# Kernel tuning notes

Hardware: AMD Instinct MI355X
Metric: run time of the kernel (lower is better)

The kernel has to match this reference:

```python
import jax, jax.numpy as jnp
import numpy as np

N_NODES = 50000
N_EDGES = 600000
D_IN = 128
HID = 128
N_SAGE = 2          # num_layers - 1
N_GRAPHS = 512
BN_EPS = 1e-5


def setup_inputs() -> dict:
    key = jax.random.key(0)
    ks = jax.random.split(key, 12)
    s = 1.0 / np.sqrt(HID)
    x = jax.random.normal(ks[0], (N_NODES, D_IN), dtype=jnp.float32)
    edge_index = jax.random.randint(ks[1], (2, N_EDGES), 0, N_NODES, dtype=jnp.int32)
    batch = jnp.sort(jax.random.randint(ks[2], (N_NODES,), 0, N_GRAPHS, dtype=jnp.int32))
    # GIN MLP: Linear(D_IN,HID) -> ReLU -> Linear(HID,HID)
    gin_w1 = jax.random.normal(ks[3], (D_IN, HID), dtype=jnp.float32) * s
    gin_b1 = jnp.zeros((HID,), jnp.float32)
    gin_w2 = jax.random.normal(ks[4], (HID, HID), dtype=jnp.float32) * s
    gin_b2 = jnp.zeros((HID,), jnp.float32)
    # SAGEConv layers: lin_l (neighbors, with bias), lin_r (root, no bias)
    sage_wl = jax.random.normal(ks[5], (N_SAGE, HID, HID), dtype=jnp.float32) * s
    sage_bl = jnp.zeros((N_SAGE, HID), jnp.float32)
    sage_wr = jax.random.normal(ks[6], (N_SAGE, HID, HID), dtype=jnp.float32) * s
    # BatchNorm per layer (3 layers)
    bn_gamma = jnp.ones((1 + N_SAGE, HID), jnp.float32)
    bn_beta = jnp.zeros((1 + N_SAGE, HID), jnp.float32)
    return {"x": x, "edge_index": edge_index, "batch": batch,
            "gin_w1": gin_w1, "gin_b1": gin_b1, "gin_w2": gin_w2, "gin_b2": gin_b2,
            "sage_wl": sage_wl, "sage_bl": sage_bl, "sage_wr": sage_wr,
            "bn_gamma": bn_gamma, "bn_beta": bn_beta}


def _batchnorm(h, gamma, beta):
    # training-mode BN over the node dimension (biased variance, as torch)
    mu = jnp.mean(h, axis=0)
    var = jnp.var(h, axis=0)
    return gamma * (h - mu) * jax.lax.rsqrt(var + BN_EPS) + beta


def reference(x, edge_index, batch, gin_w1, gin_b1, gin_w2, gin_b2,
              sage_wl, sage_bl, sage_wr, bn_gamma, bn_beta):
    n = x.shape[0]
    src, dst = edge_index[0], edge_index[1]

    # ---- Layer 0: GINConv (eps=0): mlp(x + sum_{j->i} x_j) ----
    agg = jax.ops.segment_sum(x[src], dst, num_segments=n)  # [N, D_IN]
    h = x + agg
    h = jax.nn.relu(h @ gin_w1 + gin_b1) @ gin_w2 + gin_b2
    h = jax.nn.relu(_batchnorm(h, bn_gamma[0], bn_beta[0]))
    # dropout is identity (eval mode)

    # degree for mean aggregation (shared across SAGE layers)
    deg = jax.ops.segment_sum(jnp.ones((src.shape[0],), h.dtype), dst, num_segments=n)
    inv_deg = (1.0 / jnp.maximum(deg, 1.0))[:, None]  # [N,1]

    # ---- SAGE layers: lin_l(mean_{j->i} h_j) + lin_r(h_i) ----
    for l in range(N_SAGE):
        neigh = jax.ops.segment_sum(h[src], dst, num_segments=n) * inv_deg
        h = neigh @ sage_wl[l] + sage_bl[l] + h @ sage_wr[l]
        h = jax.nn.relu(_batchnorm(h, bn_gamma[l + 1], bn_beta[l + 1]))

    # ---- global mean pool over batch ids ----
    sums = jax.ops.segment_sum(h, batch, num_segments=N_GRAPHS)  # [G, HID]
    counts = jax.ops.segment_sum(jnp.ones((n,), h.dtype), batch, num_segments=N_GRAPHS)
    return sums / jnp.maximum(counts, 1.0)[:, None]
```

## Files before the change

### kernel.cpp

```cpp
#include <hip/hip_runtime.h>

#define N_NODES 50000
#define N_EDGES 600000
#define HID 128
#define N_GRAPHS 512
#define BN_EPS 1e-5f
#define INV_N (1.0f / 50000.0f)

typedef __attribute__((ext_vector_type(8))) short bf16x8;
typedef __attribute__((ext_vector_type(4))) float f32x4;

__device__ __forceinline__ unsigned short f2b(float f) {
    unsigned u = __float_as_uint(f);
    return (unsigned short)((u + 0x7FFFu + ((u >> 16) & 1u)) >> 16);
}
__device__ __forceinline__ float b2f(unsigned short h) {
    return __uint_as_float(((unsigned)h) << 16);
}

#define CONVX_BLOCKS 6250
#define WCONV_BLOCKS 384
#define DEG_BLOCKS   2344
__global__ __launch_bounds__(256) void prep_kernel(
    const float* __restrict__ x, const float* __restrict__ gw1, const float* __restrict__ gw2,
    const float* __restrict__ swl, const float* __restrict__ swr, const int* __restrict__ dst,
    unsigned short* __restrict__ x16, unsigned short* __restrict__ wt, int* __restrict__ deg)
{
    int b = blockIdx.x;
    int t = threadIdx.x;
    if (b < CONVX_BLOCKS) {
        int gid = b * 256 + t;
        int i = gid >> 5, l = gid & 31;
        if (i >= N_NODES) return;
        int c0 = l * 4;
        float4 v = *(const float4*)(x + (size_t)i * 128 + c0);
        ushort4 o;
        o.x = f2b(v.x); o.y = f2b(v.y); o.z = f2b(v.z); o.w = f2b(v.w);
        *(ushort4*)(x16 + (size_t)i * 128 + c0) = o;
    } else if (b < CONVX_BLOCKS + WCONV_BLOCKS) {
        int gid = (b - CONVX_BLOCKS) * 256 + t;
        int m = gid >> 14;
        int e = gid & 16383;
        int k = e >> 7;
        int n = e & 127;
        const float* src = (m == 0) ? gw1 : (m == 1) ? gw2 : (m == 2) ? swl
                         : (m == 3) ? swr : (m == 4) ? (swl + 16384) : (swr + 16384);
        wt[m * 16384 + n * 128 + k] = f2b(src[k * 128 + n]);
    } else {
        int e = (b - CONVX_BLOCKS - WCONV_BLOCKS) * 256 + t;
        if (e < N_EDGES) atomicAdd(&deg[dst[e]], 1);
    }
}

#define ALLOC_BLOCKS 196
__global__ __launch_bounds__(256) void alloc_kernel(int* __restrict__ cursor,
                                                    int* __restrict__ row_beg,
                                                    float* __restrict__ inv_deg,
                                                    int* __restrict__ total,
                                                    const int* __restrict__ batch,
                                                    int* __restrict__ gstart) {
    if (blockIdx.x >= ALLOC_BLOCKS) {
        int g = (blockIdx.x - ALLOC_BLOCKS) * 256 + threadIdx.x;
        if (g > N_GRAPHS) return;
        int lo = 0, hi = N_NODES;
        while (lo < hi) {
            int mid = (lo + hi) >> 1;
            if (batch[mid] < g) lo = mid + 1; else hi = mid;
        }
        gstart[g] = lo;
        return;
    }
    __shared__ int tmp[256];
    __shared__ int base;
    int i = blockIdx.x * 256 + threadIdx.x;
    int d = (i < N_NODES) ? cursor[i] : 0;
    tmp[threadIdx.x] = d;
    __syncthreads();
#pragma unroll
    for (int off = 1; off < 256; off <<= 1) {
        int v = (threadIdx.x >= off) ? tmp[threadIdx.x - off] : 0;
        __syncthreads();
        tmp[threadIdx.x] += v;
        __syncthreads();
    }
    if (threadIdx.x == 255) base = atomicAdd(total, tmp[255]);
    __syncthreads();
    if (i < N_NODES) {
        int b = base + tmp[threadIdx.x] - d;
        row_beg[i] = b;
        cursor[i] = b;
        inv_deg[i] = 1.0f / fmaxf((float)d, 1.0f);
    }
}

__global__ void csr_fill_kernel(const int* __restrict__ src, const int* __restrict__ dst,
                                int* __restrict__ cursor, unsigned short* __restrict__ csr_src, int nE) {
    int e = blockIdx.x * blockDim.x + threadIdx.x;
    if (e < nE) {
        int pos = atomicAdd(&cursor[dst[e]], 1);
        csr_src[pos] = (unsigned short)src[e];
    }
}

#define IDXCAP 2048
template<bool AFF, bool MEAN, bool HACT>
__global__ __launch_bounds__(256) void aggregate_kernel(
    const unsigned short* __restrict__ feat,
    const int* __restrict__ row_beg, const int* __restrict__ row_end,
    const unsigned short* __restrict__ csr_src,
    const float* __restrict__ stats, const float* __restrict__ gamma,
    const float* __restrict__ beta, const float* __restrict__ inv_deg,
    unsigned short* __restrict__ agg, unsigned short* __restrict__ hact, int n)
{
    __shared__ unsigned short idxbuf[IDXCAP];
    const int t = threadIdx.x;
    const int node0 = blockIdx.x * 16;
    const int node = node0 + (t >> 4);
    const int lane = t & 15;
    const int c0 = lane * 8;

    const int last = (node0 + 15 < n) ? node0 + 15 : n - 1;
    const int ebeg = row_beg[node0];
    const int ecnt = row_end[last] - ebeg;
    const bool lds_ok = (ecnt <= IDXCAP);
    if (lds_ok) {
        for (int i = t; i < ecnt; i += 256) idxbuf[i] = csr_src[ebeg + i];
    }
    __syncthreads();
    if (node >= n) return;

    float cc[8], ss[8];
    if (AFF) {
#pragma unroll
        for (int j = 0; j < 8; j++) {
            int col = c0 + j;
            float mu = stats[col] * INV_N;
            float var = stats[128 + col] * INV_N - mu * mu;
            float rs = rsqrtf(var + BN_EPS);
            float c = gamma[col] * rs;
            cc[j] = c;
            ss[j] = beta[col] - mu * c;
        }
    }

    float a[8];
#pragma unroll
    for (int j = 0; j < 8; j++) a[j] = 0.f;

    const int beg = row_beg[node];
    const int deg = row_end[node] - beg;

    if (lds_ok) {
        const int off = beg - ebeg;
        int e = 0;
        for (; e + 7 < deg; e += 8) {
            int s[8];
#pragma unroll
            for (int u = 0; u < 8; u++) s[u] = idxbuf[off + e + u];
            bf16x8 v[8];
#pragma unroll
            for (int u = 0; u < 8; u++)
                v[u] = *(const bf16x8*)(feat + (size_t)s[u] * 128 + c0);
#pragma unroll
            for (int u = 0; u < 8; u++) {
#pragma unroll
                for (int j = 0; j < 8; j++) {
                    float tv = b2f((unsigned short)v[u][j]);
                    if (AFF) tv = fmaxf(tv * cc[j] + ss[j], 0.f);
                    a[j] += tv;
                }
            }
        }
        for (; e + 3 < deg; e += 4) {
            int s[4];
#pragma unroll
            for (int u = 0; u < 4; u++) s[u] = idxbuf[off + e + u];
            bf16x8 v[4];
#pragma unroll
            for (int u = 0; u < 4; u++)
                v[u] = *(const bf16x8*)(feat + (size_t)s[u] * 128 + c0);
#pragma unroll
            for (int u = 0; u < 4; u++) {
#pragma unroll
                for (int j = 0; j < 8; j++) {
                    float tv = b2f((unsigned short)v[u][j]);
                    if (AFF) tv = fmaxf(tv * cc[j] + ss[j], 0.f);
                    a[j] += tv;
                }
            }
        }
        for (; e < deg; e++) {
            int s0 = idxbuf[off + e];
            bf16x8 v0 = *(const bf16x8*)(feat + (size_t)s0 * 128 + c0);
#pragma unroll
            for (int j = 0; j < 8; j++) {
                float tv = b2f((unsigned short)v0[j]);
                if (AFF) tv = fmaxf(tv * cc[j] + ss[j], 0.f);
                a[j] += tv;
            }
        }
    } else {
        int e = beg, end = beg + deg;
        for (; e + 3 < end; e += 4) {
            int s0 = csr_src[e];
            int s1 = csr_src[e + 1];
            int s2 = csr_src[e + 2];
            int s3 = csr_src[e + 3];
            bf16x8 v0 = *(const bf16x8*)(feat + (size_t)s0 * 128 + c0);
            bf16x8 v1 = *(const bf16x8*)(feat + (size_t)s1 * 128 + c0);
            bf16x8 v2 = *(const bf16x8*)(feat + (size_t)s2 * 128 + c0);
            bf16x8 v3 = *(const bf16x8*)(feat + (size_t)s3 * 128 + c0);
#pragma unroll
            for (int j = 0; j < 8; j++) {
                float t0 = b2f((unsigned short)v0[j]);
                float t1 = b2f((unsigned short)v1[j]);
                float t2 = b2f((unsigned short)v2[j]);
                float t3 = b2f((unsigned short)v3[j]);
                if (AFF) {
                    t0 = fmaxf(t0 * cc[j] + ss[j], 0.f);
                    t1 = fmaxf(t1 * cc[j] + ss[j], 0.f);
                    t2 = fmaxf(t2 * cc[j] + ss[j], 0.f);
                    t3 = fmaxf(t3 * cc[j] + ss[j], 0.f);
                }
                a[j] += (t0 + t1) + (t2 + t3);
            }
        }
        for (; e < end; e++) {
            int s0 = csr_src[e];
            bf16x8 v0 = *(const bf16x8*)(feat + (size_t)s0 * 128 + c0);
#pragma unroll
            for (int j = 0; j < 8; j++) {
                float t0 = b2f((unsigned short)v0[j]);
                if (AFF) t0 = fmaxf(t0 * cc[j] + ss[j], 0.f);
                a[j] += t0;
            }
        }
    }

    if (MEAN) {
        float s = inv_deg[node];
#pragma unroll
        for (int j = 0; j < 8; j++) a[j] *= s;
    }
    bf16x8 o;
#pragma unroll
    for (int j = 0; j < 8; j++) o[j] = (short)f2b(a[j]);
    *(bf16x8*)(agg + (size_t)node * 128 + c0) = o;

    if (HACT) {
        bf16x8 v = *(const bf16x8*)(feat + (size_t)node * 128 + c0);
        bf16x8 h;
#pragma unroll
        for (int j = 0; j < 8; j++)
            h[j] = (short)f2b(fmaxf(b2f((unsigned short)v[j]) * cc[j] + ss[j], 0.f));
        *(bf16x8*)(hact + (size_t)node * 128 + c0) = h;
    }
}

__global__ __launch_bounds__(256, 2) void gemm_gin_kernel(
    const unsigned short* __restrict__ X, const unsigned short* __restrict__ AGG,
    const unsigned short* __restrict__ W1t, const unsigned short* __restrict__ W2t,
    const float* __restrict__ b1, const float* __restrict__ b2,
    float* __restrict__ stats, unsigned short* __restrict__ Cb,
    int M, int ntiles)
{
    __shared__ unsigned short t1[32][136];
    __shared__ float red[2][128];

    const int t = threadIdx.x;
    const int wave = t >> 6;
    const int lane = t & 63;
    const int colhalf = wave & 1;
    const int rowpair = wave >> 1;
    const int m16 = lane & 15;
    const int quad = lane >> 4;
    const int k0 = quad * 8;
    const int colbase = colhalf * 64;
    const int lrow = rowpair * 16 + m16;

    const bf16x8 zero8 = {0, 0, 0, 0, 0, 0, 0, 0};

    bf16x8 w1f[4][4], w2f[4][4];
#pragma unroll
    for (int ct = 0; ct < 4; ct++) {
        int col = colbase + ct * 16 + m16;
#pragma unroll
        for (int kc = 0; kc < 4; kc++) {
            w1f[ct][kc] = *(const bf16x8*)(W1t + (size_t)col * 128 + kc * 32 + k0);
            w2f[ct][kc] = *(const bf16x8*)(W2t + (size_t)col * 128 + kc * 32 + k0);
        }
    }
    f32x4 bs1[4], bs2[4];
#pragma unroll
    for (int ct = 0; ct < 4; ct++) {
        bs1[ct] = *(const f32x4*)(b1 + colbase + ct * 16 + quad * 4);
        bs2[ct] = *(const f32x4*)(b2 + colbase + ct * 16 + quad * 4);
    }

    float psum[4][4], psq[4][4];
#pragma unroll
    for (int ct = 0; ct < 4; ct++)
#pragma unroll
        for (int r = 0; r < 4; r++) { psum[ct][r] = 0.f; psq[ct][r] = 0.f; }

    for (int tile = blockIdx.x; tile < ntiles; tile += gridDim.x) {
        int arow = tile * 32 + rowpair * 16 + m16;
        bool aok = arow < M;

        bf16x8 a[4];
#pragma unroll
        for (int kc = 0; kc < 4; kc++) {
            if (aok) {
                bf16x8 vx = *(const bf16x8*)(X + (size_t)arow * 128 + kc * 32 + k0);
                bf16x8 vg = *(const bf16x8*)(AGG + (size_t)arow * 128 + kc * 32 + k0);
                bf16x8 r;
#pragma unroll
                for (int i = 0; i < 8; i++)
                    r[i] = (short)f2b(b2f((unsigned short)vx[i]) + b2f((unsigned short)vg[i]));
                a[kc] = r;
            } else {
                a[kc] = zero8;
            }
        }

        f32x4 acc[4];
#pragma unroll
        for (int ct = 0; ct < 4; ct++) acc[ct] = (f32x4){0.f, 0.f, 0.f, 0.f};
#pragma unroll
        for (int kc = 0; kc < 4; kc++)
#pragma unroll
            for (int ct = 0; ct < 4; ct++)
                acc[ct] = __builtin_amdgcn_mfma_f32_16x16x32_bf16(w1f[ct][kc], a[kc], acc[ct], 0, 0, 0);

        __syncthreads();
#pragma unroll
        for (int ct = 0; ct < 4; ct++) {
            f32x4 v = acc[ct] + bs1[ct];
            ushort4 o;
            o.x = f2b(fmaxf(v[0], 0.f));
            o.y = f2b(fmaxf(v[1], 0.f));
            o.z = f2b(fmaxf(v[2], 0.f));
            o.w = f2b(fmaxf(v[3], 0.f));
            *(ushort4*)&t1[lrow][colbase + ct * 16 + quad * 4] = o;
        }
        __syncthreads();

        bf16x8 ta[4];
#pragma unroll
        for (int kc = 0; kc < 4; kc++)
            ta[kc] = *(const bf16x8*)&t1[lrow][kc * 32 + k0];

        f32x4 acc2[4];
#pragma unroll
        for (int ct = 0; ct < 4; ct++) acc2[ct] = (f32x4){0.f, 0.f, 0.f, 0.f};
#pragma unroll
        for (int kc = 0; kc < 4; kc++)
#pragma unroll
            for (int ct = 0; ct < 4; ct++)
                acc2[ct] = __builtin_amdgcn_mfma_f32_16x16x32_bf16(w2f[ct][kc], ta[kc], acc2[ct], 0, 0, 0);

        int orow = arow;
        if (orow < M) {
#pragma unroll
            for (int ct = 0; ct < 4; ct++) {
                f32x4 v = acc2[ct] + bs2[ct];
                int col = colbase + ct * 16 + quad * 4;
#pragma unroll
                for (int r = 0; r < 4; r++) { psum[ct][r] += v[r]; psq[ct][r] += v[r] * v[r]; }
                ushort4 o;
                o.x = f2b(v[0]); o.y = f2b(v[1]); o.z = f2b(v[2]); o.w = f2b(v[3]);
                *(ushort4*)(Cb + (size_t)orow * 128 + col) = o;
            }
        }
    }

#pragma unroll
    for (int ct = 0; ct < 4; ct++)
#pragma unroll
        for (int r = 0; r < 4; r++) {
#pragma unroll
            for (int mask = 1; mask <= 8; mask <<= 1) {
                psum[ct][r] += __shfl_xor(psum[ct][r], mask, 64);
                psq[ct][r]  += __shfl_xor(psq[ct][r], mask, 64);
            }
        }
    __syncthreads();
    if (m16 == 0) {
#pragma unroll
        for (int ct = 0; ct < 4; ct++)
#pragma unroll
            for (int r = 0; r < 4; r++)
                red[rowpair][colbase + ct * 16 + quad * 4 + r] = psum[ct][r];
    }
    __syncthreads();
    if (t < 128) atomicAdd(&stats[t], red[0][t] + red[1][t]);
    __syncthreads();
    if (m16 == 0) {
#pragma unroll
        for (int ct = 0; ct < 4; ct++)
#pragma unroll
            for (int r = 0; r < 4; r++)
                red[rowpair][colbase + ct * 16 + quad * 4 + r] = psq[ct][r];
    }
    __syncthreads();
    if (t < 128) atomicAdd(&stats[128 + t], red[0][t] + red[1][t]);
}

__global__ __launch_bounds__(256) void gemm_dual_kernel(
    const unsigned short* __restrict__ A1, const unsigned short* __restrict__ A2,
    const unsigned short* __restrict__ W1t, const unsigned short* __restrict__ W2t,
    const float* __restrict__ bias, float* __restrict__ stats,
    unsigned short* __restrict__ Cb, int M, int ntiles)
{
    __shared__ float red[128];

    const int t = threadIdx.x;
    const int wave = t >> 6;
    const int lane = t & 63;
    const int m16 = lane & 15;
    const int quad = lane >> 4;
    const int k0 = quad * 8;
    const int colbase = wave * 32;

    const bf16x8 zero8 = {0, 0, 0, 0, 0, 0, 0, 0};

    bf16x8 w1f[2][4], w2f[2][4];
#pragma unroll
    for (int ct = 0; ct < 2; ct++) {
        int col = colbase + ct * 16 + m16;
#pragma unroll
        for (int kc = 0; kc < 4; kc++) {
            w1f[ct][kc] = *(const bf16x8*)(W1t + (size_t)col * 128 + kc * 32 + k0);
            w2f[ct][kc] = *(const bf16x8*)(W2t + (size_t)col * 128 + kc * 32 + k0);
        }
    }
    f32x4 bs[2];
#pragma unroll
    for (int ct = 0; ct < 2; ct++)
        bs[ct] = *(const f32x4*)(bias + colbase + ct * 16 + quad * 4);

    float psum[2][4], psq[2][4];
#pragma unroll
    for (int ct = 0; ct < 2; ct++)
#pragma unroll
        for (int r = 0; r < 4; r++) { psum[ct][r] = 0.f; psq[ct][r] = 0.f; }

    bf16x8 a1[4], a2[4], a1n[4], a2n[4];

    int tile = blockIdx.x;
    if (tile < ntiles) {
        int arow = tile * 16 + m16;
        bool aok = arow < M;
#pragma unroll
        for (int kc = 0; kc < 4; kc++) {
            a1[kc] = aok ? *(const bf16x8*)(A1 + (size_t)arow * 128 + kc * 32 + k0) : zero8;
            a2[kc] = aok ? *(const bf16x8*)(A2 + (size_t)arow * 128 + kc * 32 + k0) : zero8;
        }
    }

    for (; tile < ntiles; tile += gridDim.x) {
        int nt = tile + gridDim.x;
        if (nt < ntiles) {
            int arow = nt * 16 + m16;
            bool aok = arow < M;
#pragma unroll
            for (int kc = 0; kc < 4; kc++) {
                a1n[kc] = aok ? *(const bf16x8*)(A1 + (size_t)arow * 128 + kc * 32 + k0) : zero8;
                a2n[kc] = aok ? *(const bf16x8*)(A2 + (size_t)arow * 128 + kc * 32 + k0) : zero8;
            }
        }

        f32x4 acc[2];
        acc[0] = (f32x4){0.f, 0.f, 0.f, 0.f};
        acc[1] = (f32x4){0.f, 0.f, 0.f, 0.f};
#pragma unroll
        for (int kc = 0; kc < 4; kc++) {
#pragma unroll
            for (int ct = 0; ct < 2; ct++) {
                acc[ct] = __builtin_amdgcn_mfma_f32_16x16x32_bf16(w1f[ct][kc], a1[kc], acc[ct], 0, 0, 0);
                acc[ct] = __builtin_amdgcn_mfma_f32_16x16x32_bf16(w2f[ct][kc], a2[kc], acc[ct], 0, 0, 0);
            }
        }

        int orow = tile * 16 + m16;
        if (orow < M) {
#pragma unroll
            for (int ct = 0; ct < 2; ct++) {
                f32x4 v = acc[ct] + bs[ct];
                int col = colbase + ct * 16 + quad * 4;
#pragma unroll
                for (int r = 0; r < 4; r++) { psum[ct][r] += v[r]; psq[ct][r] += v[r] * v[r]; }
                ushort4 o;
                o.x = f2b(v[0]); o.y = f2b(v[1]); o.z = f2b(v[2]); o.w = f2b(v[3]);
                *(ushort4*)(Cb + (size_t)orow * 128 + col) = o;
            }
        }

        if (nt < ntiles) {
            a1[0] = a1n[0]; a1[1] = a1n[1]; a1[2] = a1n[2]; a1[3] = a1n[3];
            a2[0] = a2n[0]; a2[1] = a2n[1]; a2[2] = a2n[2]; a2[3] = a2n[3];
        }
    }

#pragma unroll
    for (int ct = 0; ct < 2; ct++)
#pragma unroll
        for (int r = 0; r < 4; r++) {
#pragma unroll
            for (int mask = 1; mask <= 8; mask <<= 1) {
                psum[ct][r] += __shfl_xor(psum[ct][r], mask, 64);
                psq[ct][r]  += __shfl_xor(psq[ct][r], mask, 64);
            }
        }
    if (m16 == 0) {
#pragma unroll
        for (int ct = 0; ct < 2; ct++)
#pragma unroll
            for (int r = 0; r < 4; r++)
                red[colbase + ct * 16 + quad * 4 + r] = psum[ct][r];
    }
    __syncthreads();
    if (t < 128) atomicAdd(&stats[t], red[t]);
    __syncthreads();
    if (m16 == 0) {
#pragma unroll
        for (int ct = 0; ct < 2; ct++)
#pragma unroll
            for (int r = 0; r < 4; r++)
                red[colbase + ct * 16 + quad * 4 + r] = psq[ct][r];
    }
    __syncthreads();
    if (t < 128) atomicAdd(&stats[128 + t], red[t]);
}

__global__ __launch_bounds__(128) void pool_mean_kernel(const unsigned short* __restrict__ h,
                                                        const int* __restrict__ gstart,
                                                        const float* __restrict__ stats,
                                                        const float* __restrict__ gamma,
                                                        const float* __restrict__ beta,
                                                        float* __restrict__ out) {
    __shared__ float red[8][128];
    int g = blockIdx.x;
    int t = threadIdx.x;
    int lane = t & 15, grp = t >> 4;
    int c0 = lane * 8;
    float c[8], b[8];
#pragma unroll
    for (int j = 0; j < 8; j++) {
        int col = c0 + j;
        float mu = stats[col] * INV_N;
        float var = stats[128 + col] * INV_N - mu * mu;
        float rs = rsqrtf(var + BN_EPS);
        c[j] = gamma[col] * rs;
        b[j] = beta[col] - mu * c[j];
    }
    int beg = gstart[g];
    int end = gstart[g + 1];
    float s[8];
#pragma unroll
    for (int j = 0; j < 8; j++) s[j] = 0.f;
    for (int i = beg + grp; i < end; i += 8) {
        bf16x8 v = *(const bf16x8*)(h + (size_t)i * 128 + c0);
#pragma unroll
        for (int j = 0; j < 8; j++)
            s[j] += fmaxf(b2f((unsigned short)v[j]) * c[j] + b[j], 0.f);
    }
#pragma unroll
    for (int j = 0; j < 8; j++) red[grp][c0 + j] = s[j];
    __syncthreads();
    if (t < 16) {
        float cnt = fmaxf((float)(end - beg), 1.0f);
        int cc0 = t * 8;
#pragma unroll
        for (int j = 0; j < 8; j++) {
            float tot = 0.f;
#pragma unroll
            for (int r = 0; r < 8; r++) tot += red[r][cc0 + j];
            out[(size_t)g * 128 + cc0 + j] = tot / cnt;
        }
    }
}

extern "C" void kernel_launch(void* const* d_in, const int* in_sizes, int n_in,
                              void* d_out, int out_size, void* d_ws, size_t ws_size,
                              hipStream_t stream) {
    const float* x    = (const float*)d_in[0];
    const int*   ei   = (const int*)d_in[1];
    const int*   src  = ei;
    const int*   dst  = ei + N_EDGES;
    const int*   batch = (const int*)d_in[2];
    const float* gw1  = (const float*)d_in[3];
    const float* gb1  = (const float*)d_in[4];
    const float* gw2  = (const float*)d_in[5];
    const float* gb2  = (const float*)d_in[6];
    const float* swl  = (const float*)d_in[7];
    const float* sbl  = (const float*)d_in[8];
    const float* swr  = (const float*)d_in[9];
    const float* bng  = (const float*)d_in[10];
    const float* bnb  = (const float*)d_in[11];
    float* out = (float*)d_out;

    float* ws = (float*)d_ws;
    unsigned short* x16    = (unsigned short*)(ws + 0);
    unsigned short* agg16  = (unsigned short*)(ws + 3200000);
    unsigned short* hact16 = (unsigned short*)(ws + 6400000);
    unsigned short* hpre16 = (unsigned short*)(ws + 9600000);
    unsigned short* wt     = (unsigned short*)(ws + 12800000);
    float*          inv_deg= ws + 12850000;
    int*            row_beg= (int*)(ws + 12900000);
    int*            cursor = (int*)(ws + 12950000);
    int*            total  = cursor + 50000;
    float*          stats  = (float*)(cursor + 50001);
    unsigned short* csr_src= (unsigned short*)(ws + 13100000);
    int*            gstart = (int*)(ws + 13700000);

    const int aggr_blocks = (N_NODES + 15) / 16;
    const int ntiles32 = (N_NODES + 31) / 32;
    const int ntiles16 = (N_NODES + 15) / 16;
    const int ggrid = 512;

    hipMemsetAsync(cursor, 0, (50001 + 768) * sizeof(int), stream);

    prep_kernel<<<CONVX_BLOCKS + WCONV_BLOCKS + DEG_BLOCKS, 256, 0, stream>>>(
        x, gw1, gw2, swl, swr, dst, x16, wt, cursor);

    alloc_kernel<<<ALLOC_BLOCKS + 3, 256, 0, stream>>>(cursor, row_beg, inv_deg, total, batch, gstart);
    csr_fill_kernel<<<(N_EDGES + 255) / 256, 256, 0, stream>>>(src, dst, cursor, csr_src, N_EDGES);

    aggregate_kernel<false, false, false><<<aggr_blocks, 256, 0, stream>>>(
        x16, row_beg, cursor, csr_src, nullptr, nullptr, nullptr, nullptr, agg16, nullptr, N_NODES);
    gemm_gin_kernel<<<ggrid, 256, 0, stream>>>(
        x16, agg16, wt + 0 * 16384, wt + 1 * 16384, gb1, gb2, stats + 0, hpre16, N_NODES, ntiles32);

    aggregate_kernel<true, true, true><<<aggr_blocks, 256, 0, stream>>>(
        hpre16, row_beg, cursor, csr_src, stats + 0, bng + 0 * HID, bnb + 0 * HID, inv_deg,
        agg16, hact16, N_NODES);
    gemm_dual_kernel<<<ggrid, 256, 0, stream>>>(
        agg16, hact16, wt + 2 * 16384, wt + 3 * 16384, sbl + 0 * HID, stats + 256, hpre16, N_NODES, ntiles16);

    aggregate_kernel<true, true, true><<<aggr_blocks, 256, 0, stream>>>(
        hpre16, row_beg, cursor, csr_src, stats + 256, bng + 1 * HID, bnb + 1 * HID, inv_deg,
        agg16, hact16, N_NODES);
    gemm_dual_kernel<<<ggrid, 256, 0, stream>>>(
        agg16, hact16, wt + 4 * 16384, wt + 5 * 16384, sbl + 1 * HID, stats + 512, hpre16, N_NODES, ntiles16);

    pool_mean_kernel<<<N_GRAPHS, 128, 0, stream>>>(
        hpre16, gstart, stats + 512, bng + 2 * HID, bnb + 2 * HID, out);
}
```

Measured before the change: 348.9 us.

## Fuse neighbor aggregation with GEMM per layer and shard BN stat atomics

Merges each layer's gather-aggregate kernel with its following MFMA GEMM into one persistent kernel. Each block processes 16-node groups: it gathers neighbor rows into registers, stages them in LDS, then runs the MLP or dual SAGE GEMM directly, so the intermediate agg and hact buffers are no longer written to and re-read from global memory. BatchNorm statistic atomics are spread over 8 shard copies that readers sum back together, to reduce atomic contention. In exchange, gather and GEMM run serialized within each block, with more syncthreads per group. The GIN MLP now uses 16-row tiles, and the unrolled non-LDS fallback gather loop is reduced to a simple one-edge loop.

```diff
diff --git a/kernel.cpp b/kernel.cpp
--- a/kernel.cpp
+++ b/kernel.cpp
@@ -6,6 +6,9 @@
 #define N_GRAPHS 512
 #define BN_EPS 1e-5f
 #define INV_N (1.0f / 50000.0f)
+#define NGROUPS 3125
+#define FUSED_GRID 1024
+#define IDXCAP 2048
 
 typedef __attribute__((ext_vector_type(8))) short bf16x8;
 typedef __attribute__((ext_vector_type(4))) float f32x4;
@@ -16,6 +19,13 @@
 }
 __device__ __forceinline__ float b2f(unsigned short h) {
     return __uint_as_float(((unsigned)h) << 16);
+}
+
+__device__ __forceinline__ float stats_sum(const float* __restrict__ s, int idx) {
+    float v = 0.f;
+#pragma unroll
+    for (int r = 0; r < 8; r++) v += s[r * 256 + idx];
+    return v;
 }
 
 #define CONVX_BLOCKS 6250
@@ -102,54 +112,16 @@
     }
 }
 
-#define IDXCAP 2048
-template<bool AFF, bool MEAN, bool HACT>
-__global__ __launch_bounds__(256) void aggregate_kernel(
+template<bool AFF>
+__device__ __forceinline__ void gather_row(
     const unsigned short* __restrict__ feat,
-    const int* __restrict__ row_beg, const int* __restrict__ row_end,
     const unsigned short* __restrict__ csr_src,
-    const float* __restrict__ stats, const float* __restrict__ gamma,
-    const float* __restrict__ beta, const float* __restrict__ inv_deg,
-    unsigned short* __restrict__ agg, unsigned short* __restrict__ hact, int n)
+    const unsigned short* __restrict__ idxbuf,
+    bool lds_ok, int ebeg, int beg, int deg, int c0,
+    const float (&cc)[8], const float (&ss)[8], float (&a)[8])
 {
-    __shared__ unsigned short idxbuf[IDXCAP];
-    const int t = threadIdx.x;
-    const int node0 = blockIdx.x * 16;
-    const int node = node0 + (t >> 4);
-    const int lane = t & 15;
-    const int c0 = lane * 8;
-
-    const int last = (node0 + 15 < n) ? node0 + 15 : n - 1;
-    const int ebeg = row_beg[node0];
-    const int ecnt = row_end[last] - ebeg;
-    const bool lds_ok = (ecnt <= IDXCAP);
-    if (lds_ok) {
-        for (int i = t; i < ecnt; i += 256) idxbuf[i] = csr_src[ebeg + i];
-    }
-    __syncthreads();
-    if (node >= n) return;
-
-    float cc[8], ss[8];
-    if (AFF) {
-#pragma unroll
-        for (int j = 0; j < 8; j++) {
-            int col = c0 + j;
-            float mu = stats[col] * INV_N;
-            float var = stats[128 + col] * INV_N - mu * mu;
-            float rs = rsqrtf(var + BN_EPS);
-            float c = gamma[col] * rs;
-            cc[j] = c;
-            ss[j] = beta[col] - mu * c;
-        }
-    }
-
-    float a[8];
 #pragma unroll
     for (int j = 0; j < 8; j++) a[j] = 0.f;
-
-    const int beg = row_beg[node];
-    const int deg = row_end[node] - beg;
-
     if (lds_ok) {
         const int off = beg - ebeg;
         int e = 0;
@@ -162,14 +134,13 @@
             for (int u = 0; u < 8; u++)
                 v[u] = *(const bf16x8*)(feat + (size_t)s[u] * 128 + c0);
 #pragma unroll
-            for (int u = 0; u < 8; u++) {
+            for (int u = 0; u < 8; u++)
 #pragma unroll
                 for (int j = 0; j < 8; j++) {
                     float tv = b2f((unsigned short)v[u][j]);
                     if (AFF) tv = fmaxf(tv * cc[j] + ss[j], 0.f);
                     a[j] += tv;
                 }
-            }
         }
         for (; e + 3 < deg; e += 4) {
             int s[4];
@@ -180,14 +151,13 @@
             for (int u = 0; u < 4; u++)
                 v[u] = *(const bf16x8*)(feat + (size_t)s[u] * 128 + c0);
 #pragma unroll
-            for (int u = 0; u < 4; u++) {
+            for (int u = 0; u < 4; u++)
 #pragma unroll
                 for (int j = 0; j < 8; j++) {
                     float tv = b2f((unsigned short)v[u][j]);
                     if (AFF) tv = fmaxf(tv * cc[j] + ss[j], 0.f);
                     a[j] += tv;
                 }
-            }
         }
         for (; e < deg; e++) {
             int s0 = idxbuf[off + e];
@@ -200,218 +170,30 @@
             }
         }
     } else {
-        int e = beg, end = beg + deg;
-        for (; e + 3 < end; e += 4) {
-            int s0 = csr_src[e];
-            int s1 = csr_src[e + 1];
-            int s2 = csr_src[e + 2];
-            int s3 = csr_src[e + 3];
-            bf16x8 v0 = *(const bf16x8*)(feat + (size_t)s0 * 128 + c0);
-            bf16x8 v1 = *(const bf16x8*)(feat + (size_t)s1 * 128 + c0);
-            bf16x8 v2 = *(const bf16x8*)(feat + (size_t)s2 * 128 + c0);
-            bf16x8 v3 = *(const bf16x8*)(feat + (size_t)s3 * 128 + c0);
-#pragma unroll
-            for (int j = 0; j < 8; j++) {
-                float t0 = b2f((unsigned short)v0[j]);
-                float t1 = b2f((unsigned short)v1[j]);
-                float t2 = b2f((unsigned short)v2[j]);
-                float t3 = b2f((unsigned short)v3[j]);
-                if (AFF) {
-                    t0 = fmaxf(t0 * cc[j] + ss[j], 0.f);
-                    t1 = fmaxf(t1 * cc[j] + ss[j], 0.f);
-                    t2 = fmaxf(t2 * cc[j] + ss[j], 0.f);
-                    t3 = fmaxf(t3 * cc[j] + ss[j], 0.f);
-                }
-                a[j] += (t0 + t1) + (t2 + t3);
-            }
-        }
-        for (; e < end; e++) {
+        for (int e = beg; e < beg + deg; e++) {
             int s0 = csr_src[e];
             bf16x8 v0 = *(const bf16x8*)(feat + (size_t)s0 * 128 + c0);
 #pragma unroll
             for (int j = 0; j < 8; j++) {
-                float t0 = b2f((unsigned short)v0[j]);
-                if (AFF) t0 = fmaxf(t0 * cc[j] + ss[j], 0.f);
-                a[j] += t0;
+                float tv = b2f((unsigned short)v0[j]);
+                if (AFF) tv = fmaxf(tv * cc[j] + ss[j], 0.f);
+                a[j] += tv;
             }
         }
     }
-
-    if (MEAN) {
-        float s = inv_deg[node];
-#pragma unroll
-        for (int j = 0; j < 8; j++) a[j] *= s;
-    }
-    bf16x8 o;
-#pragma unroll
-    for (int j = 0; j < 8; j++) o[j] = (short)f2b(a[j]);
-    *(bf16x8*)(agg + (size_t)node * 128 + c0) = o;
-
-    if (HACT) {
-        bf16x8 v = *(const bf16x8*)(feat + (size_t)node * 128 + c0);
-        bf16x8 h;
-#pragma unroll
-        for (int j = 0; j < 8; j++)
-            h[j] = (short)f2b(fmaxf(b2f((unsigned short)v[j]) * cc[j] + ss[j], 0.f));
-        *(bf16x8*)(hact + (size_t)node * 128 + c0) = h;
-    }
-}
-
-__global__ __launch_bounds__(256, 2) void gemm_gin_kernel(
-    const unsigned short* __restrict__ X, const unsigned short* __restrict__ AGG,
+}
+
+__global__ __launch_bounds__(256, 2) void fused_gin_kernel(
+    const unsigned short* __restrict__ X,
+    const int* __restrict__ row_beg, const int* __restrict__ row_end,
+    const unsigned short* __restrict__ csr_src,
     const unsigned short* __restrict__ W1t, const unsigned short* __restrict__ W2t,
     const float* __restrict__ b1, const float* __restrict__ b2,
-    float* __restrict__ stats, unsigned short* __restrict__ Cb,
-    int M, int ntiles)
+    float* __restrict__ stats_out, unsigned short* __restrict__ Hout, int ngroups)
 {
-    __shared__ unsigned short t1[32][136];
-    __shared__ float red[2][128];
-
-    const int t = threadIdx.x;
-    const int wave = t >> 6;
-    const int lane = t & 63;
-    const int colhalf = wave & 1;
-    const int rowpair = wave >> 1;
-    const int m16 = lane & 15;
-    const int quad = lane >> 4;
-    const int k0 = quad * 8;
-    const int colbase = colhalf * 64;
-    const int lrow = rowpair * 16 + m16;
-
-    const bf16x8 zero8 = {0, 0, 0, 0, 0, 0, 0, 0};
-
-    bf16x8 w1f[4][4], w2f[4][4];
-#pragma unroll
-    for (int ct = 0; ct < 4; ct++) {
-        int col = colbase + ct * 16 + m16;
-#pragma unroll
-        for (int kc = 0; kc < 4; kc++) {
-            w1f[ct][kc] = *(const bf16x8*)(W1t + (size_t)col * 128 + kc * 32 + k0);
-            w2f[ct][kc] = *(const bf16x8*)(W2t + (size_t)col * 128 + kc * 32 + k0);
-        }
-    }
-    f32x4 bs1[4], bs2[4];
-#pragma unroll
-    for (int ct = 0; ct < 4; ct++) {
-        bs1[ct] = *(const f32x4*)(b1 + colbase + ct * 16 + quad * 4);
-        bs2[ct] = *(const f32x4*)(b2 + colbase + ct * 16 + quad * 4);
-    }
-
-    float psum[4][4], psq[4][4];
-#pragma unroll
-    for (int ct = 0; ct < 4; ct++)
-#pragma unroll
-        for (int r = 0; r < 4; r++) { psum[ct][r] = 0.f; psq[ct][r] = 0.f; }
-
-    for (int tile = blockIdx.x; tile < ntiles; tile += gridDim.x) {
-        int arow = tile * 32 + rowpair * 16 + m16;
-        bool aok = arow < M;
-
-        bf16x8 a[4];
-#pragma unroll
-        for (int kc = 0; kc < 4; kc++) {
-            if (aok) {
-                bf16x8 vx = *(const bf16x8*)(X + (size_t)arow * 128 + kc * 32 + k0);
-                bf16x8 vg = *(const bf16x8*)(AGG + (size_t)arow * 128 + kc * 32 + k0);
-                bf16x8 r;
-#pragma unroll
-                for (int i = 0; i < 8; i++)
-                    r[i] = (short)f2b(b2f((unsigned short)vx[i]) + b2f((unsigned short)vg[i]));
-                a[kc] = r;
-            } else {
-                a[kc] = zero8;
-            }
-        }
-
-        f32x4 acc[4];
-#pragma unroll
-        for (int ct = 0; ct < 4; ct++) acc[ct] = (f32x4){0.f, 0.f, 0.f, 0.f};
-#pragma unroll
-        for (int kc = 0; kc < 4; kc++)
-#pragma unroll
-            for (int ct = 0; ct < 4; ct++)
-                acc[ct] = __builtin_amdgcn_mfma_f32_16x16x32_bf16(w1f[ct][kc], a[kc], acc[ct], 0, 0, 0);
-
-        __syncthreads();
-#pragma unroll
-        for (int ct = 0; ct < 4; ct++) {
-            f32x4 v = acc[ct] + bs1[ct];
-            ushort4 o;
-            o.x = f2b(fmaxf(v[0], 0.f));
-            o.y = f2b(fmaxf(v[1], 0.f));
-            o.z = f2b(fmaxf(v[2], 0.f));
-            o.w = f2b(fmaxf(v[3], 0.f));
-            *(ushort4*)&t1[lrow][colbase + ct * 16 + quad * 4] = o;
-        }
-        __syncthreads();
-
-        bf16x8 ta[4];
-#pragma unroll
-        for (int kc = 0; kc < 4; kc++)
-            ta[kc] = *(const bf16x8*)&t1[lrow][kc * 32 + k0];
-
-        f32x4 acc2[4];
-#pragma unroll
-        for (int ct = 0; ct < 4; ct++) acc2[ct] = (f32x4){0.f, 0.f, 0.f, 0.f};
-#pragma unroll
-        for (int kc = 0; kc < 4; kc++)
-#pragma unroll
-            for (int ct = 0; ct < 4; ct++)
-                acc2[ct] = __builtin_amdgcn_mfma_f32_16x16x32_bf16(w2f[ct][kc], ta[kc], acc2[ct], 0, 0, 0);
-
-        int orow = arow;
-        if (orow < M) {
-#pragma unroll
-            for (int ct = 0; ct < 4; ct++) {
-                f32x4 v = acc2[ct] + bs2[ct];
-                int col = colbase + ct * 16 + quad * 4;
-#pragma unroll
-                for (int r = 0; r < 4; r++) { psum[ct][r] += v[r]; psq[ct][r] += v[r] * v[r]; }
-                ushort4 o;
-                o.x = f2b(v[0]); o.y = f2b(v[1]); o.z = f2b(v[2]); o.w = f2b(v[3]);
-                *(ushort4*)(Cb + (size_t)orow * 128 + col) = o;
-            }
-        }
-    }
-
-#pragma unroll
-    for (int ct = 0; ct < 4; ct++)
-#pragma unroll
-        for (int r = 0; r < 4; r++) {
-#pragma unroll
-            for (int mask = 1; mask <= 8; mask <<= 1) {
-                psum[ct][r] += __shfl_xor(psum[ct][r], mask, 64);
-                psq[ct][r]  += __shfl_xor(psq[ct][r], mask, 64);
-            }
-        }
-    __syncthreads();
-    if (m16 == 0) {
-#pragma unroll
-        for (int ct = 0; ct < 4; ct++)
-#pragma unroll
-            for (int r = 0; r < 4; r++)
-                red[rowpair][colbase + ct * 16 + quad * 4 + r] = psum[ct][r];
-    }
-    __syncthreads();
-    if (t < 128) atomicAdd(&stats[t], red[0][t] + red[1][t]);
-    __syncthreads();
-    if (m16 == 0) {
-#pragma unroll
-        for (int ct = 0; ct < 4; ct++)
-#pragma unroll
-            for (int r = 0; r < 4; r++)
-                red[rowpair][colbase + ct * 16 + quad * 4 + r] = psq[ct][r];
-    }
-    __syncthreads();
-    if (t < 128) atomicAdd(&stats[128 + t], red[0][t] + red[1][t]);
-}
-
-__global__ __launch_bounds__(256) void gemm_dual_kernel(
-    const unsigned short* __restrict__ A1, const unsigned short* __restrict__ A2,
-    const unsigned short* __restrict__ W1t, const unsigned short* __restrict__ W2t,
-    const float* __restrict__ bias, float* __restrict__ stats,
-    unsigned short* __restrict__ Cb, int M, int ntiles)
-{
+    __shared__ unsigned short idxbuf[IDXCAP];
+    __shared__ unsigned short aT[16][136];
+    __shared__ unsigned short t1[16][136];
     __shared__ float red[128];
 
     const int t = threadIdx.x;
@@ -421,8 +203,8 @@
     const int quad = lane >> 4;
     const int k0 = quad * 8;
     const int colbase = wave * 32;
-
-    const bf16x8 zero8 = {0, 0, 0, 0, 0, 0, 0, 0};
+    const int nslot = t >> 4;
+    const int c0 = (t & 15) * 8;
 
     bf16x8 w1f[2][4], w2f[2][4];
 #pragma unroll
@@ -434,103 +216,267 @@
             w2f[ct][kc] = *(const bf16x8*)(W2t + (size_t)col * 128 + kc * 32 + k0);
         }
     }
-    f32x4 bs[2];
+    f32x4 bs1[2], bs2[2];
+#pragma unroll
+    for (int ct = 0; ct < 2; ct++) {
+        bs1[ct] = *(const f32x4*)(b1 + colbase + ct * 16 + quad * 4);
+        bs2[ct] = *(const f32x4*)(b2 + colbase + ct * 16 + quad * 4);
+    }
+
+    float psum[2][4], psq[2][4];
 #pragma unroll
     for (int ct = 0; ct < 2; ct++)
-        bs[ct] = *(const f32x4*)(bias + colbase + ct * 16 + quad * 4);
-
-    float psum[2][4], psq[2][4];
-#pragma unroll
-    for (int ct = 0; ct < 2; ct++)
 #pragma unroll
         for (int r = 0; r < 4; r++) { psum[ct][r] = 0.f; psq[ct][r] = 0.f; }
 
-    bf16x8 a1[4], a2[4], a1n[4], a2n[4];
-
-    int tile = blockIdx.x;
-    if (tile < ntiles) {
-        int arow = tile * 16 + m16;
-        bool aok = arow < M;
-#pragma unroll
-        for (int kc = 0; kc < 4; kc++) {
-            a1[kc] = aok ? *(const bf16x8*)(A1 + (size_t)arow * 128 + kc * 32 + k0) : zero8;
-            a2[kc] = aok ? *(const bf16x8*)(A2 + (size_t)arow * 128 + kc * 32 + k0) : zero8;
-        }
-    }
-
-    for (; tile < ntiles; tile += gridDim.x) {
-        int nt = tile + gridDim.x;
-        if (nt < ntiles) {
-            int arow = nt * 16 + m16;
-            bool aok = arow < M;
-#pragma unroll
-            for (int kc = 0; kc < 4; kc++) {
-                a1n[kc] = aok ? *(const bf16x8*)(A1 + (size_t)arow * 128 + kc * 32 + k0) : zero8;
-                a2n[kc] = aok ? *(const bf16x8*)(A2 + (size_t)arow * 128 + kc * 32 + k0) : zero8;
-            }
-        }
-
+    float dcc[8], dss[8];
+#pragma unroll
+    for (int j = 0; j < 8; j++) { dcc[j] = 0.f; dss[j] = 0.f; }
+
+    for (int g = blockIdx.x; g < ngroups; g += gridDim.x) {
+        const int node0 = g * 16;
+        const int node = node0 + nslot;
+        const int ebeg = row_beg[node0];
+        const int ecnt = row_end[node0 + 15] - ebeg;
+        const bool lds_ok = (ecnt <= IDXCAP);
+        if (lds_ok)
+            for (int i = t; i < ecnt; i += 256) idxbuf[i] = csr_src[ebeg + i];
+        bf16x8 vself = *(const bf16x8*)(X + (size_t)node * 128 + c0);
+        const int beg = row_beg[node];
+        const int deg = row_end[node] - beg;
+        __syncthreads();
+
+        float a[8];
+        gather_row<false>(X, csr_src, idxbuf, lds_ok, ebeg, beg, deg, c0, dcc, dss, a);
+
+        bf16x8 arow;
+#pragma unroll
+        for (int j = 0; j < 8; j++)
+            arow[j] = (short)f2b(a[j] + b2f((unsigned short)vself[j]));
+        *(bf16x8*)&aT[nslot][c0] = arow;
+        __syncthreads();
+
+        bf16x8 af[4];
+#pragma unroll
+        for (int kc = 0; kc < 4; kc++)
+            af[kc] = *(const bf16x8*)&aT[m16][kc * 32 + k0];
         f32x4 acc[2];
         acc[0] = (f32x4){0.f, 0.f, 0.f, 0.f};
         acc[1] = (f32x4){0.f, 0.f, 0.f, 0.f};
 #pragma unroll
-        for (int kc = 0; kc < 4; kc++) {
-#pragma unroll
-            for (int ct = 0; ct < 2; ct++) {
-                acc[ct] = __builtin_amdgcn_mfma_f32_16x16x32_bf16(w1f[ct][kc], a1[kc], acc[ct], 0, 0, 0);
-                acc[ct] = __builtin_amdgcn_mfma_f32_16x16x32_bf16(w2f[ct][kc], a2[kc], acc[ct], 0, 0, 0);
-            }
-        }
-
-        int orow = tile * 16 + m16;
-        if (orow < M) {
-#pragma unroll
-            for (int ct = 0; ct < 2; ct++) {
-                f32x4 v = acc[ct] + bs[ct];
-                int col = colbase + ct * 16 + quad * 4;
-#pragma unroll
-                for (int r = 0; r < 4; r++) { psum[ct][r] += v[r]; psq[ct][r] += v[r] * v[r]; }
-                ushort4 o;
-                o.x = f2b(v[0]); o.y = f2b(v[1]); o.z = f2b(v[2]); o.w = f2b(v[3]);
-                *(ushort4*)(Cb + (size_t)orow * 128 + col) = o;
-            }
-        }
-
-        if (nt < ntiles) {
-            a1[0] = a1n[0]; a1[1] = a1n[1]; a1[2] = a1n[2]; a1[3] = a1n[3];
-            a2[0] = a2n[0]; a2[1] = a2n[1]; a2[2] = a2n[2]; a2[3] = a2n[3];
+        for (int kc = 0; kc < 4; kc++)
+#pragma unroll
+            for (int ct = 0; ct < 2; ct++)
+                acc[ct] = __builtin_amdgcn_mfma_f32_16x16x32_bf16(w1f[ct][kc], af[kc], acc[ct], 0, 0, 0);
+#pragma unroll
+        for (int ct = 0; ct < 2; ct++) {
+            f32x4 v = acc[ct] + bs1[ct];
+            ushort4 o;
+            o.x = f2b(fmaxf(v[0], 0.f));
+            o.y = f2b(fmaxf(v[1], 0.f));
+            o.z = f2b(fmaxf(v[2], 0.f));
+            o.w = f2b(fmaxf(v[3], 0.f));
+            *(ushort4*)&t1[m16][colbase + ct * 16 + quad * 4] = o;
+        }
+        __syncthreads();
+
+        bf16x8 tf[4];
+#pragma unroll
+        for (int kc = 0; kc < 4; kc++)
+            tf[kc] = *(const bf16x8*)&t1[m16][kc * 32 + k0];
+        f32x4 acc2[2];
+        acc2[0] = (f32x4){0.f, 0.f, 0.f, 0.f};
+        acc2[1] = (f32x4){0.f, 0.f, 0.f, 0.f};
+#pragma unroll
+        for (int kc = 0; kc < 4; kc++)
+#pragma unroll
+            for (int ct = 0; ct < 2; ct++)
+                acc2[ct] = __builtin_amdgcn_mfma_f32_16x16x32_bf16(w2f[ct][kc], tf[kc], acc2[ct], 0, 0, 0);
+
+        const int orow = node0 + m16;
+#pragma unroll
+        for (int ct = 0; ct < 2; ct++) {
+            f32x4 v = acc2[ct] + bs2[ct];
+            int col = colbase + ct * 16 + quad * 4;
+#pragma unroll
+            for (int r = 0; r < 4; r++) { psum[ct][r] += v[r]; psq[ct][r] += v[r] * v[r]; }
+            ushort4 o;
+            o.x = f2b(v[0]); o.y = f2b(v[1]); o.z = f2b(v[2]); o.w = f2b(v[3]);
+            *(ushort4*)(Hout + (size_t)orow * 128 + col) = o;
         }
     }
 
 #pragma unroll
     for (int ct = 0; ct < 2; ct++)
 #pragma unroll
-        for (int r = 0; r < 4; r++) {
+        for (int r = 0; r < 4; r++)
 #pragma unroll
             for (int mask = 1; mask <= 8; mask <<= 1) {
                 psum[ct][r] += __shfl_xor(psum[ct][r], mask, 64);
                 psq[ct][r]  += __shfl_xor(psq[ct][r], mask, 64);
             }
-        }
-    if (m16 == 0) {
+    __syncthreads();
+    if (m16 == 0)
 #pragma unroll
         for (int ct = 0; ct < 2; ct++)
 #pragma unroll
             for (int r = 0; r < 4; r++)
                 red[colbase + ct * 16 + quad * 4 + r] = psum[ct][r];
-    }
-    __syncthreads();
-    if (t < 128) atomicAdd(&stats[t], red[t]);
-    __syncthreads();
-    if (m16 == 0) {
+    __syncthreads();
+    if (t < 128) atomicAdd(&stats_out[(blockIdx.x & 7) * 256 + t], red[t]);
+    __syncthreads();
+    if (m16 == 0)
 #pragma unroll
         for (int ct = 0; ct < 2; ct++)
 #pragma unroll
             for (int r = 0; r < 4; r++)
                 red[colbase + ct * 16 + quad * 4 + r] = psq[ct][r];
-    }
-    __syncthreads();
-    if (t < 128) atomicAdd(&stats[128 + t], red[t]);
+    __syncthreads();
+    if (t < 128) atomicAdd(&stats_out[(blockIdx.x & 7) * 256 + 128 + t], red[t]);
+}
+
+__global__ __launch_bounds__(256, 2) void fused_sage_kernel(
+    const unsigned short* __restrict__ Hin,
+    const int* __restrict__ row_beg, const int* __restrict__ row_end,
+    const unsigned short* __restrict__ csr_src,
+    const float* __restrict__ stats_in, const float* __restrict__ gamma,
+    const float* __restrict__ beta, const float* __restrict__ inv_deg,
+    const unsigned short* __restrict__ Wlt, const unsigned short* __restrict__ Wrt,
+    const float* __restrict__ bias, float* __restrict__ stats_out,
+    unsigned short* __restrict__ Hout, int ngroups)
+{
+    __shared__ unsigned short idxbuf[IDXCAP];
+    __shared__ unsigned short aT[16][136];
+    __shared__ unsigned short hT[16][136];
+    __shared__ float red[128];
+
+    const int t = threadIdx.x;
+    const int wave = t >> 6;
+    const int lane = t & 63;
+    const int m16 = lane & 15;
+    const int quad = lane >> 4;
+    const int k0 = quad * 8;
+    const int colbase = wave * 32;
+    const int nslot = t >> 4;
+    const int c0 = (t & 15) * 8;
+
+    float cc[8], ss[8];
+#pragma unroll
+    for (int j = 0; j < 8; j++) {
+        int col = c0 + j;
+        float mu = stats_sum(stats_in, col) * INV_N;
+        float var = stats_sum(stats_in, 128 + col) * INV_N - mu * mu;
+        float rs = rsqrtf(var + BN_EPS);
+        float c = gamma[col] * rs;
+        cc[j] = c;
+        ss[j] = beta[col] - mu * c;
+    }
+
+    bf16x8 wl[2][4], wr[2][4];
+#pragma unroll
+    for (int ct = 0; ct < 2; ct++) {
+        int col = colbase + ct * 16 + m16;
+#pragma unroll
+        for (int kc = 0; kc < 4; kc++) {
+            wl[ct][kc] = *(const bf16x8*)(Wlt + (size_t)col * 128 + kc * 32 + k0);
+            wr[ct][kc] = *(const bf16x8*)(Wrt + (size_t)col * 128 + kc * 32 + k0);
+        }
+    }
+    f32x4 bs[2];
+#pragma unroll
+    for (int ct = 0; ct < 2; ct++)
+        bs[ct] = *(const f32x4*)(bias + colbase + ct * 16 + quad * 4);
+
+    float psum[2][4], psq[2][4];
+#pragma unroll
+    for (int ct = 0; ct < 2; ct++)
+#pragma unroll
+        for (int r = 0; r < 4; r++) { psum[ct][r] = 0.f; psq[ct][r] = 0.f; }
+
+    for (int g = blockIdx.x; g < ngroups; g += gridDim.x) {
+        const int node0 = g * 16;
+        const int node = node0 + nslot;
+        const int ebeg = row_beg[node0];
+        const int ecnt = row_end[node0 + 15] - ebeg;
+        const bool lds_ok = (ecnt <= IDXCAP);
+        if (lds_ok)
+            for (int i = t; i < ecnt; i += 256) idxbuf[i] = csr_src[ebeg + i];
+        bf16x8 vself = *(const bf16x8*)(Hin + (size_t)node * 128 + c0);
+        const float sc = inv_deg[node];
+        const int beg = row_beg[node];
+        const int deg = row_end[node] - beg;
+        __syncthreads();
+
+        float a[8];
+        gather_row<true>(Hin, csr_src, idxbuf, lds_ok, ebeg, beg, deg, c0, cc, ss, a);
+
+        bf16x8 arow, hrow;
+#pragma unroll
+        for (int j = 0; j < 8; j++) {
+            arow[j] = (short)f2b(a[j] * sc);
+            hrow[j] = (short)f2b(fmaxf(b2f((unsigned short)vself[j]) * cc[j] + ss[j], 0.f));
+        }
+        *(bf16x8*)&aT[nslot][c0] = arow;
+        *(bf16x8*)&hT[nslot][c0] = hrow;
+        __syncthreads();
+
+        bf16x8 a1[4], a2[4];
+#pragma unroll
+        for (int kc = 0; kc < 4; kc++) {
+            a1[kc] = *(const bf16x8*)&aT[m16][kc * 32 + k0];
+            a2[kc] = *(const bf16x8*)&hT[m16][kc * 32 + k0];
+        }
+        f32x4 acc[2];
+        acc[0] = (f32x4){0.f, 0.f, 0.f, 0.f};
+        acc[1] = (f32x4){0.f, 0.f, 0.f, 0.f};
+#pragma unroll
+        for (int kc = 0; kc < 4; kc++)
+#pragma unroll
+            for (int ct = 0; ct < 2; ct++) {
+                acc[ct] = __builtin_amdgcn_mfma_f32_16x16x32_bf16(wl[ct][kc], a1[kc], acc[ct], 0, 0, 0);
+                acc[ct] = __builtin_amdgcn_mfma_f32_16x16x32_bf16(wr[ct][kc], a2[kc], acc[ct], 0, 0, 0);
+            }
+
+        const int orow = node0 + m16;
+#pragma unroll
+        for (int ct = 0; ct < 2; ct++) {
+            f32x4 v = acc[ct] + bs[ct];
+            int col = colbase + ct * 16 + quad * 4;
+#pragma unroll
+            for (int r = 0; r < 4; r++) { psum[ct][r] += v[r]; psq[ct][r] += v[r] * v[r]; }
+            ushort4 o;
+            o.x = f2b(v[0]); o.y = f2b(v[1]); o.z = f2b(v[2]); o.w = f2b(v[3]);
+            *(ushort4*)(Hout + (size_t)orow * 128 + col) = o;
+        }
+    }
+
+#pragma unroll
+    for (int ct = 0; ct < 2; ct++)
+#pragma unroll
+        for (int r = 0; r < 4; r++)
+#pragma unroll
+            for (int mask = 1; mask <= 8; mask <<= 1) {
+                psum[ct][r] += __shfl_xor(psum[ct][r], mask, 64);
+                psq[ct][r]  += __shfl_xor(psq[ct][r], mask, 64);
+            }
+    __syncthreads();
+    if (m16 == 0)
+#pragma unroll
+        for (int ct = 0; ct < 2; ct++)
+#pragma unroll
+            for (int r = 0; r < 4; r++)
+                red[colbase + ct * 16 + quad * 4 + r] = psum[ct][r];
+    __syncthreads();
+    if (t < 128) atomicAdd(&stats_out[(blockIdx.x & 7) * 256 + t], red[t]);
+    __syncthreads();
+    if (m16 == 0)
+#pragma unroll
+        for (int ct = 0; ct < 2; ct++)
+#pragma unroll
+            for (int r = 0; r < 4; r++)
+                red[colbase + ct * 16 + quad * 4 + r] = psq[ct][r];
+    __syncthreads();
+    if (t < 128) atomicAdd(&stats_out[(blockIdx.x & 7) * 256 + 128 + t], red[t]);
 }
 
 __global__ __launch_bounds__(128) void pool_mean_kernel(const unsigned short* __restrict__ h,
@@ -548,8 +494,8 @@
 #pragma unroll
     for (int j = 0; j < 8; j++) {
         int col = c0 + j;
-        float mu = stats[col] * INV_N;
-        float var = stats[128 + col] * INV_N - mu * mu;
+        float mu = stats_sum(stats, col) * INV_N;
+        float var = stats_sum(stats, 128 + col) * INV_N - mu * mu;
         float rs = rsqrtf(var + BN_EPS);
         c[j] = gamma[col] * rs;
         b[j] = beta[col] - mu * c[j];
@@ -602,9 +548,8 @@
 
     float* ws = (float*)d_ws;
     unsigned short* x16    = (unsigned short*)(ws + 0);
-    unsigned short* agg16  = (unsigned short*)(ws + 3200000);
-    unsigned short* hact16 = (unsigned short*)(ws + 6400000);
-    unsigned short* hpre16 = (unsigned short*)(ws + 9600000);
+    unsigned short* h_a    = (unsigned short*)(ws + 3200000);
+    unsigned short* h_b    = (unsigned short*)(ws + 6400000);
     unsigned short* wt     = (unsigned short*)(ws + 12800000);
     float*          inv_deg= ws + 12850000;
     int*            row_beg= (int*)(ws + 12900000);
@@ -614,12 +559,7 @@
     unsigned short* csr_src= (unsigned short*)(ws + 13100000);
     int*            gstart = (int*)(ws + 13700000);
 
-    const int aggr_blocks = (N_NODES + 15) / 16;
-    const int ntiles32 = (N_NODES + 31) / 32;
-    const int ntiles16 = (N_NODES + 15) / 16;
-    const int ggrid = 512;
-
-    hipMemsetAsync(cursor, 0, (50001 + 768) * sizeof(int), stream);
+    hipMemsetAsync(cursor, 0, (50001 + 3 * 8 * 256) * sizeof(int), stream);
 
     prep_kernel<<<CONVX_BLOCKS + WCONV_BLOCKS + DEG_BLOCKS, 256, 0, stream>>>(
         x, gw1, gw2, swl, swr, dst, x16, wt, cursor);
@@ -627,23 +567,18 @@
     alloc_kernel<<<ALLOC_BLOCKS + 3, 256, 0, stream>>>(cursor, row_beg, inv_deg, total, batch, gstart);
     csr_fill_kernel<<<(N_EDGES + 255) / 256, 256, 0, stream>>>(src, dst, cursor, csr_src, N_EDGES);
 
-    aggregate_kernel<false, false, false><<<aggr_blocks, 256, 0, stream>>>(
-        x16, row_beg, cursor, csr_src, nullptr, nullptr, nullptr, nullptr, agg16, nullptr, N_NODES);
-    gemm_gin_kernel<<<ggrid, 256, 0, stream>>>(
-        x16, agg16, wt + 0 * 16384, wt + 1 * 16384, gb1, gb2, stats + 0, hpre16, N_NODES, ntiles32);
-
-    aggregate_kernel<true, true, true><<<aggr_blocks, 256, 0, stream>>>(
-        hpre16, row_beg, cursor, csr_src, stats + 0, bng + 0 * HID, bnb + 0 * HID, inv_deg,
-        agg16, hact16, N_NODES);
-    gemm_dual_kernel<<<ggrid, 256, 0, stream>>>(
-        agg16, hact16, wt + 2 * 16384, wt + 3 * 16384, sbl + 0 * HID, stats + 256, hpre16, N_NODES, ntiles16);
-
-    aggregate_kernel<true, true, true><<<aggr_blocks, 256, 0, stream>>>(
-        hpre16, row_beg, cursor, csr_src, stats + 256, bng + 1 * HID, bnb + 1 * HID, inv_deg,
-        agg16, hact16, N_NODES);
-    gemm_dual_kernel<<<ggrid, 256, 0, stream>>>(
-        agg16, hact16, wt + 4 * 16384, wt + 5 * 16384, sbl + 1 * HID, stats + 512, hpre16, N_NODES, ntiles16);
+    fused_gin_kernel<<<FUSED_GRID, 256, 0, stream>>>(
+        x16, row_beg, cursor, csr_src, wt + 0 * 16384, wt + 1 * 16384,
+        gb1, gb2, stats + 0 * 2048, h_a, NGROUPS);
+
+    fused_sage_kernel<<<FUSED_GRID, 256, 0, stream>>>(
+        h_a, row_beg, cursor, csr_src, stats + 0 * 2048, bng + 0 * HID, bnb + 0 * HID,
+        inv_deg, wt + 2 * 16384, wt + 3 * 16384, sbl + 0 * HID, stats + 1 * 2048, h_b, NGROUPS);
+
+    fused_sage_kernel<<<FUSED_GRID, 256, 0, stream>>>(
+        h_b, row_beg, cursor, csr_src, stats + 1 * 2048, bng + 1 * HID, bnb + 1 * HID,
+        inv_deg, wt + 4 * 16384, wt + 5 * 16384, sbl + 1 * HID, stats + 2 * 2048, h_a, NGROUPS);
 
     pool_mean_kernel<<<N_GRAPHS, 128, 0, stream>>>(
-        hpre16, gstart, stats + 512, bng + 2 * HID, bnb + 2 * HID, out);
-}
+        h_a, gstart, stats + 2 * 2048, bng + 2 * HID, bnb + 2 * HID, out);
+}
```

Result: faster. 313.7 us (-10.1%).
